# Kernel optimization log

Measured on AMD Instinct MI355X. Metric: run time of the kernel, lower is better.

The kernel has to match this reference:

```python
import jax, jax.numpy as jnp
import numpy as np

NEG_SLOPE = 0.2
BN_EPS = 1e-5
SM_EPS = 1e-16


def gatv2_conv(x, src, dst, num_nodes, Wl, bl, Wr, br, att, bias, concat):
    # x: [N, Fin]; att: [H, C]
    H, C = att.shape
    xl = (x @ Wl + bl).reshape(-1, H, C)  # source-side (x_j), lin_l
    xr = (x @ Wr + br).reshape(-1, H, C)  # target-side (x_i), lin_r
    e = jax.nn.leaky_relu(xl[src] + xr[dst], NEG_SLOPE)          # [E, H, C]
    logits = jnp.einsum('ehc,hc->eh', e, att)                    # [E, H]
    m = jax.ops.segment_max(logits, dst, num_segments=num_nodes)  # [N, H]
    expv = jnp.exp(logits - m[dst])
    denom = jax.ops.segment_sum(expv, dst, num_segments=num_nodes)
    alpha = expv / (denom[dst] + SM_EPS)                          # [E, H]
    msg = xl[src] * alpha[:, :, None]                             # [E, H, C]
    out = jax.ops.segment_sum(msg, dst, num_segments=num_nodes)   # [N, H, C]
    out = out.reshape(num_nodes, H * C) if concat else out.mean(axis=1)
    return out + bias


def batchnorm(x, gamma, beta):
    mean = x.mean(axis=0)
    var = x.var(axis=0)  # biased, as torch uses for normalization
    return gamma * (x - mean) * jax.lax.rsqrt(var + BN_EPS) + beta


def setup_inputs() -> dict:
    key = jax.random.key(0)
    ks = jax.random.split(key, 16)
    N, E = 50000, 800000
    Fin, Hid, Out, H = 128, 64, 64, 4
    s = 0.05
    inp = {
        'x': jax.random.normal(ks[0], (N, Fin), jnp.float32),
        'edge_index': jax.random.randint(ks[1], (2, E), 0, N, jnp.int64),
        # conv1 (heads=4, concat=False)
        'Wl1': jax.random.normal(ks[2], (Fin, H * Hid), jnp.float32) * s,
        'bl1': jnp.zeros((H * Hid,), jnp.float32),
        'Wr1': jax.random.normal(ks[3], (Fin, H * Hid), jnp.float32) * s,
        'br1': jnp.zeros((H * Hid,), jnp.float32),
        'att1': jax.random.normal(ks[4], (H, Hid), jnp.float32) * s,
        'bias1': jnp.zeros((Hid,), jnp.float32),
        'g1': jnp.ones((Hid,), jnp.float32),
        'beta1': jnp.zeros((Hid,), jnp.float32),
        # conv2 (heads=1, concat=True -> same as single head)
        'Wl2': jax.random.normal(ks[5], (Hid, Out), jnp.float32) * s,
        'bl2': jnp.zeros((Out,), jnp.float32),
        'Wr2': jax.random.normal(ks[6], (Hid, Out), jnp.float32) * s,
        'br2': jnp.zeros((Out,), jnp.float32),
        'att2': jax.random.normal(ks[7], (1, Out), jnp.float32) * s,
        'bias2': jnp.zeros((Out,), jnp.float32),
        'g2': jnp.ones((Out,), jnp.float32),
        'beta2': jnp.zeros((Out,), jnp.float32),
    }
    return inp


def reference(x, edge_index, Wl1, bl1, Wr1, br1, att1, bias1, g1, beta1,
              Wl2, bl2, Wr2, br2, att2, bias2, g2, beta2):
    N = x.shape[0]
    loops = jnp.arange(N, dtype=edge_index.dtype)  # PyG add_self_loops=True
    src = jnp.concatenate([edge_index[0], loops])
    dst = jnp.concatenate([edge_index[1], loops])
    h = gatv2_conv(x, src, dst, N, Wl1, bl1, Wr1, br1, att1, bias1, concat=False)
    h = jax.nn.relu(batchnorm(h, g1, beta1))  # dropout = identity (eval)
    h = gatv2_conv(h, src, dst, N, Wl2, bl2, Wr2, br2, att2, bias2, concat=True)
    h = jax.nn.relu(batchnorm(h, g2, beta2))
    return h
```

## Files before the change

kernel.cpp:

```cpp
#include <hip/hip_runtime.h>
#include <hip/hip_bf16.h>
#include <math.h>

#define TPB 256

typedef __attribute__((ext_vector_type(8))) short bfrag8;
typedef __attribute__((ext_vector_type(4))) float f32x4;

static __device__ __forceinline__ float bf2f(unsigned int u) {
  union { unsigned int i; float f; } c; c.i = u << 16; return c.f;
}
static __device__ __forceinline__ unsigned short f2bf(float f) {
  union { float f; unsigned int i; } c; c.f = f;
  unsigned int lsb = (c.i >> 16) & 1u;
  return (unsigned short)((c.i + 0x7fffu + lsb) >> 16);
}
static __device__ __forceinline__ float lrelu(float v) {
  return v > 0.f ? v : 0.2f * v;
}

__global__ void k_deg(const int* __restrict__ ei, int E, int ET, int* __restrict__ deg) {
  int e = blockIdx.x * blockDim.x + threadIdx.x;
  if (e >= ET) return;
  int dst = (e < E) ? ei[E + e] : (e - E);
  atomicAdd(&deg[dst], 1);
}

__global__ void k_scan1(const int* __restrict__ deg, int N, int* __restrict__ bsum) {
  __shared__ int sm[TPB];
  int i = blockIdx.x * TPB + threadIdx.x;
  sm[threadIdx.x] = (i < N) ? deg[i] : 0;
  __syncthreads();
  for (int d = TPB / 2; d > 0; d >>= 1) {
    if (threadIdx.x < d) sm[threadIdx.x] += sm[threadIdx.x + d];
    __syncthreads();
  }
  if (threadIdx.x == 0) bsum[blockIdx.x] = sm[0];
}

__global__ void k_scan2(const int* __restrict__ bsum, int SB, int* __restrict__ bpre,
                        int* __restrict__ rowoff, int N) {
  __shared__ int sm[TPB];
  int v = (threadIdx.x < SB) ? bsum[threadIdx.x] : 0;
  sm[threadIdx.x] = v;
  __syncthreads();
  for (int d = 1; d < TPB; d <<= 1) {
    int t = (threadIdx.x >= d) ? sm[threadIdx.x - d] : 0;
    __syncthreads();
    sm[threadIdx.x] += t;
    __syncthreads();
  }
  if (threadIdx.x < SB) bpre[threadIdx.x] = sm[threadIdx.x] - v;
  if (threadIdx.x == SB - 1) rowoff[N] = sm[SB - 1];
}

__global__ void k_scan3(const int* __restrict__ deg, const int* __restrict__ bpre,
                        int N, int* __restrict__ rowoff, int* __restrict__ cursor) {
  __shared__ int sm[TPB];
  int i = blockIdx.x * TPB + threadIdx.x;
  int v = (i < N) ? deg[i] : 0;
  sm[threadIdx.x] = v;
  __syncthreads();
  for (int d = 1; d < TPB; d <<= 1) {
    int t = (threadIdx.x >= d) ? sm[threadIdx.x - d] : 0;
    __syncthreads();
    sm[threadIdx.x] += t;
    __syncthreads();
  }
  if (i < N) {
    int off = bpre[blockIdx.x] + sm[threadIdx.x] - v;
    rowoff[i] = off;
    cursor[i] = off;
  }
}

__global__ void k_fill(const int* __restrict__ ei, int E, int ET,
                       int* __restrict__ cursor, int* __restrict__ csrc) {
  int e = blockIdx.x * blockDim.x + threadIdx.x;
  if (e >= ET) return;
  int src, dst;
  if (e < E) { src = ei[e]; dst = ei[E + e]; } else { src = dst = e - E; }
  int pos = atomicAdd(&cursor[dst], 1);
  csrc[pos] = src;
}

__global__ void k_gemm_mfma(const float* __restrict__ A,
                            const float* __restrict__ W0, const float* __restrict__ b0,
                            const float* __restrict__ W1, const float* __restrict__ b1,
                            unsigned short* __restrict__ out0, unsigned short* __restrict__ out1,
                            int M, int K, int Nc, const float* __restrict__ affine) {
  __shared__ short As[64 * 128];
  __shared__ short Bls[64 * 128];
  __shared__ short Brs[64 * 128];
  const int r0 = blockIdx.x * 64, n0 = blockIdx.y * 64;
  const int tid = threadIdx.x;
  const int Kb = K * 2;

  const int kq = K >> 2;
  for (int idx = tid; idx < 16 * K; idx += TPB) {
    int row = idx / kq, c4 = idx - row * kq;
    int gr = r0 + row;
    float4 v = make_float4(0.f, 0.f, 0.f, 0.f);
    if (gr < M) v = *(const float4*)(A + (size_t)gr * K + c4 * 4);
    if (affine) {
      int c = c4 * 4;
      v.x = fmaxf(v.x * affine[c + 0] + affine[64 + c + 0], 0.f);
      v.y = fmaxf(v.y * affine[c + 1] + affine[64 + c + 1], 0.f);
      v.z = fmaxf(v.z * affine[c + 2] + affine[64 + c + 2], 0.f);
      v.w = fmaxf(v.w * affine[c + 3] + affine[64 + c + 3], 0.f);
    }
    ushort4 pk; pk.x = f2bf(v.x); pk.y = f2bf(v.y); pk.z = f2bf(v.z); pk.w = f2bf(v.w);
    int kb = (c4 * 8) ^ ((row & 7) << 4);
    *(ushort4*)((char*)As + row * Kb + kb) = pk;
  }
  for (int idx = tid; idx < 16 * K; idx += TPB) {
    int c = idx & 63, k4 = (idx >> 6) << 2;
    const float* p0 = W0 + (size_t)k4 * Nc + n0 + c;
    const float* p1 = W1 + (size_t)k4 * Nc + n0 + c;
    ushort4 pk0, pk1;
    pk0.x = f2bf(p0[0]); pk0.y = f2bf(p0[Nc]); pk0.z = f2bf(p0[2 * Nc]); pk0.w = f2bf(p0[3 * Nc]);
    pk1.x = f2bf(p1[0]); pk1.y = f2bf(p1[Nc]); pk1.z = f2bf(p1[2 * Nc]); pk1.w = f2bf(p1[3 * Nc]);
    int kb = (k4 * 2) ^ ((c & 7) << 4);
    *(ushort4*)((char*)Bls + c * Kb + kb) = pk0;
    *(ushort4*)((char*)Brs + c * Kb + kb) = pk1;
  }
  __syncthreads();

  const int w = tid >> 6, lane = tid & 63;
  const int arow = w * 16 + (lane & 15);
  const int l16 = (lane >> 4) << 3;
  f32x4 accL[4], accR[4];
#pragma unroll
  for (int i = 0; i < 4; ++i) { accL[i] = (f32x4)0.f; accR[i] = (f32x4)0.f; }
  for (int k0 = 0; k0 < K; k0 += 32) {
    int kb = (k0 + l16) * 2;
    bfrag8 af = *(bfrag8*)((char*)As + arow * Kb + (kb ^ ((arow & 7) << 4)));
#pragma unroll
    for (int cf = 0; cf < 4; ++cf) {
      int col = cf * 16 + (lane & 15);
      int cb = col * Kb + (kb ^ ((col & 7) << 4));
      bfrag8 bl = *(bfrag8*)((char*)Bls + cb);
      accL[cf] = __builtin_amdgcn_mfma_f32_16x16x32_bf16(af, bl, accL[cf], 0, 0, 0);
      bfrag8 br = *(bfrag8*)((char*)Brs + cb);
      accR[cf] = __builtin_amdgcn_mfma_f32_16x16x32_bf16(af, br, accR[cf], 0, 0, 0);
    }
  }
  const int rbase = r0 + w * 16 + ((lane >> 4) << 2);
  const int cbase = n0 + (lane & 15);
#pragma unroll
  for (int cf = 0; cf < 4; ++cf) {
    int gcol = cbase + cf * 16;
    float bb0 = b0[gcol], bb1 = b1[gcol];
#pragma unroll
    for (int r = 0; r < 4; ++r) {
      int grow = rbase + r;
      if (grow < M) {
        out0[(size_t)grow * Nc + gcol] = f2bf(accL[cf][r] + bb0);
        out1[(size_t)grow * Nc + gcol] = f2bf(accR[cf][r] + bb1);
      }
    }
  }
}

__global__ void k_gat1(const unsigned short* __restrict__ xl,
                       const unsigned short* __restrict__ xr,
                       const int* __restrict__ rowoff, const int* __restrict__ csrc,
                       const float* __restrict__ att, const float* __restrict__ bias,
                       float* __restrict__ out, int N) {
  int node = (blockIdx.x * blockDim.x + threadIdx.x) >> 6;
  int lane = threadIdx.x & 63;
  if (node >= N) return;
  int l4 = lane * 4;
  uint2 rv = *(const uint2*)(xr + (size_t)node * 256 + l4);
  float xr0 = bf2f(rv.x & 0xffffu), xr1 = bf2f(rv.x >> 16);
  float xr2 = bf2f(rv.y & 0xffffu), xr3 = bf2f(rv.y >> 16);
  float4 at = *(const float4*)(att + l4);
  int beg = rowoff[node], end = rowoff[node + 1];
  float s = 0.f, a0 = 0.f, a1 = 0.f, a2 = 0.f, a3 = 0.f;
  int k = beg;
  for (; k + 4 <= end; k += 4) {
    int srcs[4];
#pragma unroll
    for (int u = 0; u < 4; ++u) srcs[u] = csrc[k + u];
    uint2 vv[4];
#pragma unroll
    for (int u = 0; u < 4; ++u) vv[u] = *(const uint2*)(xl + (size_t)srcs[u] * 256 + l4);
    float xs[4][4], ps[4];
#pragma unroll
    for (int u = 0; u < 4; ++u) {
      xs[u][0] = bf2f(vv[u].x & 0xffffu); xs[u][1] = bf2f(vv[u].x >> 16);
      xs[u][2] = bf2f(vv[u].y & 0xffffu); xs[u][3] = bf2f(vv[u].y >> 16);
      ps[u] = lrelu(xs[u][0] + xr0) * at.x + lrelu(xs[u][1] + xr1) * at.y
            + lrelu(xs[u][2] + xr2) * at.z + lrelu(xs[u][3] + xr3) * at.w;
    }
#pragma unroll
    for (int u = 0; u < 4; ++u) {
      ps[u] += __shfl_xor(ps[u], 1); ps[u] += __shfl_xor(ps[u], 2);
      ps[u] += __shfl_xor(ps[u], 4); ps[u] += __shfl_xor(ps[u], 8);
    }
#pragma unroll
    for (int u = 0; u < 4; ++u) {
      float w = __expf(ps[u]);
      s += w;
      a0 += w * xs[u][0]; a1 += w * xs[u][1];
      a2 += w * xs[u][2]; a3 += w * xs[u][3];
    }
  }
  for (; k < end; ++k) {
    int src = csrc[k];
    uint2 v = *(const uint2*)(xl + (size_t)src * 256 + l4);
    float x0 = bf2f(v.x & 0xffffu), x1 = bf2f(v.x >> 16);
    float x2 = bf2f(v.y & 0xffffu), x3 = bf2f(v.y >> 16);
    float p = lrelu(x0 + xr0) * at.x + lrelu(x1 + xr1) * at.y
            + lrelu(x2 + xr2) * at.z + lrelu(x3 + xr3) * at.w;
    p += __shfl_xor(p, 1); p += __shfl_xor(p, 2);
    p += __shfl_xor(p, 4); p += __shfl_xor(p, 8);
    float w = __expf(p);
    s += w;
    a0 += w * x0; a1 += w * x1; a2 += w * x2; a3 += w * x3;
  }
  float inv = 1.f / (s + 1e-16f);
  a0 *= inv; a1 *= inv; a2 *= inv; a3 *= inv;
  a0 += __shfl_xor(a0, 16); a0 += __shfl_xor(a0, 32);
  a1 += __shfl_xor(a1, 16); a1 += __shfl_xor(a1, 32);
  a2 += __shfl_xor(a2, 16); a2 += __shfl_xor(a2, 32);
  a3 += __shfl_xor(a3, 16); a3 += __shfl_xor(a3, 32);
  if (lane < 16) {
    float4 o;
    o.x = a0 * 0.25f + bias[l4 + 0];
    o.y = a1 * 0.25f + bias[l4 + 1];
    o.z = a2 * 0.25f + bias[l4 + 2];
    o.w = a3 * 0.25f + bias[l4 + 3];
    *(float4*)(out + (size_t)node * 64 + l4) = o;
  }
}

__global__ void k_gat2(const unsigned short* __restrict__ xl,
                       const unsigned short* __restrict__ xr,
                       const int* __restrict__ rowoff, const int* __restrict__ csrc,
                       const float* __restrict__ att, const float* __restrict__ bias,
                       float* __restrict__ out, int N) {
  int node = (blockIdx.x * blockDim.x + threadIdx.x) >> 6;
  int lane = threadIdx.x & 63;
  if (node >= N) return;
  int grp = lane >> 4, c4 = (lane & 15) * 4;
  uint2 rv = *(const uint2*)(xr + (size_t)node * 64 + c4);
  float xr0 = bf2f(rv.x & 0xffffu), xr1 = bf2f(rv.x >> 16);
  float xr2 = bf2f(rv.y & 0xffffu), xr3 = bf2f(rv.y >> 16);
  float4 at = *(const float4*)(att + c4);
  int beg = rowoff[node], end = rowoff[node + 1];
  int iters = (end - beg + 3) >> 2;
  float s = 0.f, a0 = 0.f, a1 = 0.f, a2 = 0.f, a3 = 0.f;
  for (int it = 0; it < iters; ++it) {
    int kk = beg + it * 4 + grp;
    bool ok = kk < end;
    int src = ok ? csrc[kk] : 0;
    uint2 v = *(const uint2*)(xl + (size_t)src * 64 + c4);
    float x0 = bf2f(v.x & 0xffffu), x1 = bf2f(v.x >> 16);
    float x2 = bf2f(v.y & 0xffffu), x3 = bf2f(v.y >> 16);
    float p = lrelu(x0 + xr0) * at.x + lrelu(x1 + xr1) * at.y
            + lrelu(x2 + xr2) * at.z + lrelu(x3 + xr3) * at.w;
    p += __shfl_xor(p, 1); p += __shfl_xor(p, 2);
    p += __shfl_xor(p, 4); p += __shfl_xor(p, 8);
    float w = ok ? __expf(p) : 0.f;
    s += w;
    a0 += w * x0; a1 += w * x1; a2 += w * x2; a3 += w * x3;
  }
  s  += __shfl_xor(s, 16);  s  += __shfl_xor(s, 32);
  a0 += __shfl_xor(a0, 16); a0 += __shfl_xor(a0, 32);
  a1 += __shfl_xor(a1, 16); a1 += __shfl_xor(a1, 32);
  a2 += __shfl_xor(a2, 16); a2 += __shfl_xor(a2, 32);
  a3 += __shfl_xor(a3, 16); a3 += __shfl_xor(a3, 32);
  if (lane < 16) {
    float inv = 1.f / (s + 1e-16f);
    float4 o;
    o.x = a0 * inv + bias[c4 + 0];
    o.y = a1 * inv + bias[c4 + 1];
    o.z = a2 * inv + bias[c4 + 2];
    o.w = a3 * inv + bias[c4 + 3];
    *(float4*)(out + (size_t)node * 64 + c4) = o;
  }
}

__global__ void k_bnstat(const float* __restrict__ in, int N, float* __restrict__ part) {
  __shared__ float sm[TPB], sq[TPB];
  int col = threadIdx.x & 63;
  int rq = threadIdx.x >> 6;
  float s = 0.f, q = 0.f;
  for (int r = blockIdx.x * 4 + rq; r < N; r += gridDim.x * 4) {
    float v = in[(size_t)r * 64 + col];
    s += v; q += v * v;
  }
  sm[threadIdx.x] = s; sq[threadIdx.x] = q;
  __syncthreads();
  if (threadIdx.x < 64) {
    s = sm[threadIdx.x] + sm[threadIdx.x + 64] + sm[threadIdx.x + 128] + sm[threadIdx.x + 192];
    q = sq[threadIdx.x] + sq[threadIdx.x + 64] + sq[threadIdx.x + 128] + sq[threadIdx.x + 192];
    part[(size_t)blockIdx.x * 128 + threadIdx.x] = s;
    part[(size_t)blockIdx.x * 128 + 64 + threadIdx.x] = q;
  }
}

__global__ void k_bnfin(const float* __restrict__ part, int B, int N,
                        const float* __restrict__ g, const float* __restrict__ beta,
                        float* __restrict__ ab) {
  int c = threadIdx.x;
  float s = 0.f, q = 0.f;
  for (int b = 0; b < B; ++b) {
    s += part[(size_t)b * 128 + c];
    q += part[(size_t)b * 128 + 64 + c];
  }
  float mean = s / (float)N;
  float var = q / (float)N - mean * mean;
  float a = g[c] * rsqrtf(var + 1e-5f);
  ab[c] = a;
  ab[64 + c] = beta[c] - mean * a;
}

__global__ void k_bnapply(const float* __restrict__ in, const float* __restrict__ ab,
                          float* __restrict__ out, int total4) {
  int idx = blockIdx.x * blockDim.x + threadIdx.x;
  if (idx >= total4) return;
  float4 v = *(const float4*)(in + (size_t)idx * 4);
  int c0 = (idx & 15) * 4;
  v.x = fmaxf(v.x * ab[c0 + 0] + ab[64 + c0 + 0], 0.f);
  v.y = fmaxf(v.y * ab[c0 + 1] + ab[64 + c0 + 1], 0.f);
  v.z = fmaxf(v.z * ab[c0 + 2] + ab[64 + c0 + 2], 0.f);
  v.w = fmaxf(v.w * ab[c0 + 3] + ab[64 + c0 + 3], 0.f);
  *(float4*)(out + (size_t)idx * 4) = v;
}

extern "C" void kernel_launch(void* const* d_in, const int* in_sizes, int n_in,
                              void* d_out, int out_size, void* d_ws, size_t ws_size,
                              hipStream_t stream) {
  const float* x     = (const float*)d_in[0];
  const int*   ei    = (const int*)d_in[1];
  const float* Wl1   = (const float*)d_in[2];
  const float* bl1   = (const float*)d_in[3];
  const float* Wr1   = (const float*)d_in[4];
  const float* br1   = (const float*)d_in[5];
  const float* att1  = (const float*)d_in[6];
  const float* bias1 = (const float*)d_in[7];
  const float* g1    = (const float*)d_in[8];
  const float* be1   = (const float*)d_in[9];
  const float* Wl2   = (const float*)d_in[10];
  const float* bl2   = (const float*)d_in[11];
  const float* Wr2   = (const float*)d_in[12];
  const float* br2   = (const float*)d_in[13];
  const float* att2  = (const float*)d_in[14];
  const float* bias2 = (const float*)d_in[15];
  const float* g2    = (const float*)d_in[16];
  const float* be2   = (const float*)d_in[17];
  float* out = (float*)d_out;

  const int N  = in_sizes[0] / 128;
  const int E  = in_sizes[1] / 2;
  const int ET = E + N;
  const int SB = (N + TPB - 1) / TPB;

  char* p = (char*)d_ws;
  auto take = [&](size_t b) { char* q = p; p += (b + 255) & ~(size_t)255; return q; };

  unsigned short* xl1 = (unsigned short*)take((size_t)N * 256 * 2);
  unsigned short* xr1 = (unsigned short*)take((size_t)N * 256 * 2);
  unsigned short* xl2 = (unsigned short*)take((size_t)N * 64 * 2);
  unsigned short* xr2 = (unsigned short*)take((size_t)N * 64 * 2);
  float* out1 = (float*)take((size_t)N * 64 * 4);
  int* deg    = (int*)take((size_t)N * 4);
  int* rowoff = (int*)take((size_t)(N + 1) * 4);
  int* cursor = (int*)take((size_t)N * 4);
  int* csrc   = (int*)take((size_t)ET * 4);
  int* bsum   = (int*)take((size_t)SB * 4);
  int* bpre   = (int*)take((size_t)SB * 4);
  float* part = (float*)take((size_t)128 * 128 * 4);
  float* ab1  = (float*)take(128 * 4);
  float* ab2  = (float*)take(128 * 4);
  (void)ws_size; (void)n_in; (void)out_size;

  int egrid = (ET + TPB - 1) / TPB;
  int ngrid = (N + 3) / 4;
  int mtile = (N + 63) / 64;
  int total4 = N * 16;

  hipMemsetAsync(deg, 0, (size_t)N * 4, stream);
  k_deg<<<egrid, TPB, 0, stream>>>(ei, E, ET, deg);
  k_scan1<<<SB, TPB, 0, stream>>>(deg, N, bsum);
  k_scan2<<<1, TPB, 0, stream>>>(bsum, SB, bpre, rowoff, N);
  k_scan3<<<SB, TPB, 0, stream>>>(deg, bpre, N, rowoff, cursor);
  k_fill<<<egrid, TPB, 0, stream>>>(ei, E, ET, cursor, csrc);

  k_gemm_mfma<<<dim3(mtile, 4), TPB, 0, stream>>>(x, Wl1, bl1, Wr1, br1, xl1, xr1,
                                                  N, 128, 256, nullptr);
  k_gat1<<<ngrid, TPB, 0, stream>>>(xl1, xr1, rowoff, csrc, att1, bias1, out1, N);
  k_bnstat<<<128, TPB, 0, stream>>>(out1, N, part);
  k_bnfin<<<1, 64, 0, stream>>>(part, 128, N, g1, be1, ab1);

  k_gemm_mfma<<<dim3(mtile, 1), TPB, 0, stream>>>(out1, Wl2, bl2, Wr2, br2, xl2, xr2,
                                                  N, 64, 64, ab1);
  k_gat2<<<ngrid, TPB, 0, stream>>>(xl2, xr2, rowoff, csrc, att2, bias2, out, N);
  k_bnstat<<<128, TPB, 0, stream>>>(out, N, part);
  k_bnfin<<<1, 64, 0, stream>>>(part, 128, N, g2, be2, ab2);
  k_bnapply<<<(total4 + TPB - 1) / TPB, TPB, 0, stream>>>(out, ab2, out, total4);
}
```

Measured before the change: 406.9 us.

## Pad CSR rows to multiples of four, pre-transpose weights, restructure GEMM and GAT kernels

Weight matrices are now converted once to transposed bf16 inside the degree-count kernel. Each GEMM block loads its A tile once and loops over all output column tiles, instead of launching separate column blocks that reload A and convert weights. CSR rows are padded to a multiple of four so the GAT kernels can use int4 index loads and a masked tail, and the separate scan2 kernel is removed by having each scan3 block reduce the prior block sums itself. Lane reductions use DPP row rotates instead of shuffles, and the bnstat grid is doubled. In exchange, padding needs a larger zeroed csrc buffer, and the GEMM with K=128 now runs fewer blocks, each doing serial column loops.

```diff
diff --git a/kernel.cpp b/kernel.cpp
--- a/kernel.cpp
+++ b/kernel.cpp
@@ -15,21 +15,52 @@
   unsigned int lsb = (c.i >> 16) & 1u;
   return (unsigned short)((c.i + 0x7fffu + lsb) >> 16);
 }
-static __device__ __forceinline__ float lrelu(float v) {
-  return v > 0.f ? v : 0.2f * v;
-}
-
-__global__ void k_deg(const int* __restrict__ ei, int E, int ET, int* __restrict__ deg) {
-  int e = blockIdx.x * blockDim.x + threadIdx.x;
-  if (e >= ET) return;
-  int dst = (e < E) ? ei[E + e] : (e - E);
-  atomicAdd(&deg[dst], 1);
+
+#define DPP_ROR(v, C) __int_as_float(__builtin_amdgcn_update_dpp( \
+    __float_as_int(v), __float_as_int(v), (C), 0xf, 0xf, false))
+static __device__ __forceinline__ float red16(float p) {
+  p += DPP_ROR(p, 0x121);
+  p += DPP_ROR(p, 0x122);
+  p += DPP_ROR(p, 0x124);
+  p += DPP_ROR(p, 0x128);
+  return p;
+}
+
+__global__ void k_deg_prep(const int* __restrict__ ei, int E, int ET, int* __restrict__ deg,
+                           const float* __restrict__ Wl1, const float* __restrict__ Wr1,
+                           const float* __restrict__ Wl2, const float* __restrict__ Wr2,
+                           unsigned short* __restrict__ wt1l, unsigned short* __restrict__ wt1r,
+                           unsigned short* __restrict__ wt2l, unsigned short* __restrict__ wt2r,
+                           int egrid) {
+  int b = blockIdx.x;
+  if (b < egrid) {
+    int e = b * TPB + threadIdx.x;
+    if (e < ET) {
+      int dst = (e < E) ? ei[E + e] : (e - E);
+      atomicAdd(&deg[dst], 1);
+    }
+  } else {
+    int i = (b - egrid) * TPB + threadIdx.x;
+    if (i < 32768) {
+      int c = i >> 7, k = i & 127;
+      wt1l[i] = f2bf(Wl1[(size_t)k * 256 + c]);
+    } else if (i < 65536) {
+      int j = i - 32768; int c = j >> 7, k = j & 127;
+      wt1r[j] = f2bf(Wr1[(size_t)k * 256 + c]);
+    } else if (i < 69632) {
+      int j = i - 65536; int c = j >> 6, k = j & 63;
+      wt2l[j] = f2bf(Wl2[(size_t)k * 64 + c]);
+    } else if (i < 73728) {
+      int j = i - 69632; int c = j >> 6, k = j & 63;
+      wt2r[j] = f2bf(Wr2[(size_t)k * 64 + c]);
+    }
+  }
 }
 
 __global__ void k_scan1(const int* __restrict__ deg, int N, int* __restrict__ bsum) {
   __shared__ int sm[TPB];
   int i = blockIdx.x * TPB + threadIdx.x;
-  sm[threadIdx.x] = (i < N) ? deg[i] : 0;
+  sm[threadIdx.x] = (i < N) ? ((deg[i] + 3) & ~3) : 0;
   __syncthreads();
   for (int d = TPB / 2; d > 0; d >>= 1) {
     if (threadIdx.x < d) sm[threadIdx.x] += sm[threadIdx.x + d];
@@ -38,37 +69,30 @@
   if (threadIdx.x == 0) bsum[blockIdx.x] = sm[0];
 }
 
-__global__ void k_scan2(const int* __restrict__ bsum, int SB, int* __restrict__ bpre,
-                        int* __restrict__ rowoff, int N) {
+__global__ void k_scan3(const int* __restrict__ deg, const int* __restrict__ bsum,
+                        int SB, int N, int* __restrict__ rowoff, int* __restrict__ cursor) {
   __shared__ int sm[TPB];
-  int v = (threadIdx.x < SB) ? bsum[threadIdx.x] : 0;
+  int pv = (threadIdx.x < blockIdx.x) ? bsum[threadIdx.x] : 0;
+  sm[threadIdx.x] = pv;
+  __syncthreads();
+  for (int dd = TPB / 2; dd > 0; dd >>= 1) {
+    if (threadIdx.x < dd) sm[threadIdx.x] += sm[threadIdx.x + dd];
+    __syncthreads();
+  }
+  int base = sm[0];
+  __syncthreads();
+  int i = blockIdx.x * TPB + threadIdx.x;
+  int v = (i < N) ? ((deg[i] + 3) & ~3) : 0;
   sm[threadIdx.x] = v;
   __syncthreads();
-  for (int d = 1; d < TPB; d <<= 1) {
-    int t = (threadIdx.x >= d) ? sm[threadIdx.x - d] : 0;
+  for (int dd = 1; dd < TPB; dd <<= 1) {
+    int t = (threadIdx.x >= dd) ? sm[threadIdx.x - dd] : 0;
     __syncthreads();
     sm[threadIdx.x] += t;
     __syncthreads();
   }
-  if (threadIdx.x < SB) bpre[threadIdx.x] = sm[threadIdx.x] - v;
-  if (threadIdx.x == SB - 1) rowoff[N] = sm[SB - 1];
-}
-
-__global__ void k_scan3(const int* __restrict__ deg, const int* __restrict__ bpre,
-                        int N, int* __restrict__ rowoff, int* __restrict__ cursor) {
-  __shared__ int sm[TPB];
-  int i = blockIdx.x * TPB + threadIdx.x;
-  int v = (i < N) ? deg[i] : 0;
-  sm[threadIdx.x] = v;
-  __syncthreads();
-  for (int d = 1; d < TPB; d <<= 1) {
-    int t = (threadIdx.x >= d) ? sm[threadIdx.x - d] : 0;
-    __syncthreads();
-    sm[threadIdx.x] += t;
-    __syncthreads();
-  }
   if (i < N) {
-    int off = bpre[blockIdx.x] + sm[threadIdx.x] - v;
+    int off = base + sm[threadIdx.x] - v;
     rowoff[i] = off;
     cursor[i] = off;
   }
@@ -84,21 +108,26 @@
   csrc[pos] = src;
 }
 
-__global__ void k_gemm_mfma(const float* __restrict__ A,
-                            const float* __restrict__ W0, const float* __restrict__ b0,
-                            const float* __restrict__ W1, const float* __restrict__ b1,
+__global__ void k_gemm_mfma(const float* __restrict__ A, const float* __restrict__ affine,
+                            const unsigned short* __restrict__ Wt0, const float* __restrict__ b0,
+                            const unsigned short* __restrict__ Wt1, const float* __restrict__ b1,
                             unsigned short* __restrict__ out0, unsigned short* __restrict__ out1,
-                            int M, int K, int Nc, const float* __restrict__ affine) {
-  __shared__ short As[64 * 128];
-  __shared__ short Bls[64 * 128];
-  __shared__ short Brs[64 * 128];
-  const int r0 = blockIdx.x * 64, n0 = blockIdx.y * 64;
+                            int M, int K, int Nc) {
+  extern __shared__ short lds[];
+  short* As = lds;
+  short* Bls = lds + 64 * K;
+  short* Brs = lds + 128 * K;
+  const int r0 = blockIdx.x * 64;
   const int tid = threadIdx.x;
   const int Kb = K * 2;
-
-  const int kq = K >> 2;
-  for (int idx = tid; idx < 16 * K; idx += TPB) {
-    int row = idx / kq, c4 = idx - row * kq;
+  const int w = tid >> 6, lane = tid & 63;
+  const int arow = w * 16 + (lane & 15);
+  const int l16 = (lane >> 4) << 3;
+  const int rbase0 = r0 + w * 16 + ((lane >> 4) << 2);
+
+  const int fpr = K >> 2;
+  for (int idx = tid; idx < 64 * fpr; idx += TPB) {
+    int row = idx / fpr, c4 = idx - row * fpr;
     int gr = r0 + row;
     float4 v = make_float4(0.f, 0.f, 0.f, 0.f);
     if (gr < M) v = *(const float4*)(A + (size_t)gr * K + c4 * 4);
@@ -113,111 +142,127 @@
     int kb = (c4 * 8) ^ ((row & 7) << 4);
     *(ushort4*)((char*)As + row * Kb + kb) = pk;
   }
-  for (int idx = tid; idx < 16 * K; idx += TPB) {
-    int c = idx & 63, k4 = (idx >> 6) << 2;
-    const float* p0 = W0 + (size_t)k4 * Nc + n0 + c;
-    const float* p1 = W1 + (size_t)k4 * Nc + n0 + c;
-    ushort4 pk0, pk1;
-    pk0.x = f2bf(p0[0]); pk0.y = f2bf(p0[Nc]); pk0.z = f2bf(p0[2 * Nc]); pk0.w = f2bf(p0[3 * Nc]);
-    pk1.x = f2bf(p1[0]); pk1.y = f2bf(p1[Nc]); pk1.z = f2bf(p1[2 * Nc]); pk1.w = f2bf(p1[3 * Nc]);
-    int kb = (k4 * 2) ^ ((c & 7) << 4);
-    *(ushort4*)((char*)Bls + c * Kb + kb) = pk0;
-    *(ushort4*)((char*)Brs + c * Kb + kb) = pk1;
-  }
-  __syncthreads();
-
-  const int w = tid >> 6, lane = tid & 63;
-  const int arow = w * 16 + (lane & 15);
-  const int l16 = (lane >> 4) << 3;
-  f32x4 accL[4], accR[4];
-#pragma unroll
-  for (int i = 0; i < 4; ++i) { accL[i] = (f32x4)0.f; accR[i] = (f32x4)0.f; }
-  for (int k0 = 0; k0 < K; k0 += 32) {
-    int kb = (k0 + l16) * 2;
-    bfrag8 af = *(bfrag8*)((char*)As + arow * Kb + (kb ^ ((arow & 7) << 4)));
+
+  const int cpr = K >> 3;
+  for (int nt = 0; nt < Nc; nt += 64) {
+    __syncthreads();
+    for (int idx = tid; idx < 64 * cpr; idx += TPB) {
+      int c = idx / cpr, k8 = (idx - c * cpr) * 8;
+      int kb = (k8 * 2) ^ ((c & 7) << 4);
+      uint4 w0 = *(const uint4*)(Wt0 + (size_t)(nt + c) * K + k8);
+      *(uint4*)((char*)Bls + c * Kb + kb) = w0;
+      uint4 w1 = *(const uint4*)(Wt1 + (size_t)(nt + c) * K + k8);
+      *(uint4*)((char*)Brs + c * Kb + kb) = w1;
+    }
+    __syncthreads();
+
+    f32x4 accL[4], accR[4];
+#pragma unroll
+    for (int i = 0; i < 4; ++i) { accL[i] = (f32x4)0.f; accR[i] = (f32x4)0.f; }
+    for (int k0 = 0; k0 < K; k0 += 32) {
+      int kb = (k0 + l16) * 2;
+      bfrag8 af = *(bfrag8*)((char*)As + arow * Kb + (kb ^ ((arow & 7) << 4)));
+#pragma unroll
+      for (int cf = 0; cf < 4; ++cf) {
+        int col = cf * 16 + (lane & 15);
+        int cb = col * Kb + (kb ^ ((col & 7) << 4));
+        bfrag8 bl = *(bfrag8*)((char*)Bls + cb);
+        accL[cf] = __builtin_amdgcn_mfma_f32_16x16x32_bf16(af, bl, accL[cf], 0, 0, 0);
+        bfrag8 br = *(bfrag8*)((char*)Brs + cb);
+        accR[cf] = __builtin_amdgcn_mfma_f32_16x16x32_bf16(af, br, accR[cf], 0, 0, 0);
+      }
+    }
+    const int cbase = nt + (lane & 15);
 #pragma unroll
     for (int cf = 0; cf < 4; ++cf) {
-      int col = cf * 16 + (lane & 15);
-      int cb = col * Kb + (kb ^ ((col & 7) << 4));
-      bfrag8 bl = *(bfrag8*)((char*)Bls + cb);
-      accL[cf] = __builtin_amdgcn_mfma_f32_16x16x32_bf16(af, bl, accL[cf], 0, 0, 0);
-      bfrag8 br = *(bfrag8*)((char*)Brs + cb);
-      accR[cf] = __builtin_amdgcn_mfma_f32_16x16x32_bf16(af, br, accR[cf], 0, 0, 0);
-    }
-  }
-  const int rbase = r0 + w * 16 + ((lane >> 4) << 2);
-  const int cbase = n0 + (lane & 15);
-#pragma unroll
-  for (int cf = 0; cf < 4; ++cf) {
-    int gcol = cbase + cf * 16;
-    float bb0 = b0[gcol], bb1 = b1[gcol];
-#pragma unroll
-    for (int r = 0; r < 4; ++r) {
-      int grow = rbase + r;
-      if (grow < M) {
-        out0[(size_t)grow * Nc + gcol] = f2bf(accL[cf][r] + bb0);
-        out1[(size_t)grow * Nc + gcol] = f2bf(accR[cf][r] + bb1);
+      int gcol = cbase + cf * 16;
+      float bb0 = b0[gcol], bb1 = b1[gcol];
+#pragma unroll
+      for (int r = 0; r < 4; ++r) {
+        int grow = rbase0 + r;
+        if (grow < M) {
+          out0[(size_t)grow * Nc + gcol] = f2bf(accL[cf][r] + bb0);
+          out1[(size_t)grow * Nc + gcol] = f2bf(accR[cf][r] + bb1);
+        }
       }
     }
   }
 }
 
-__global__ void k_gat1(const unsigned short* __restrict__ xl,
-                       const unsigned short* __restrict__ xr,
-                       const int* __restrict__ rowoff, const int* __restrict__ csrc,
-                       const float* __restrict__ att, const float* __restrict__ bias,
-                       float* __restrict__ out, int N) {
-  int node = (blockIdx.x * blockDim.x + threadIdx.x) >> 6;
+__global__ __launch_bounds__(TPB) void k_gat1(
+    const unsigned short* __restrict__ xl, const unsigned short* __restrict__ xr,
+    const int* __restrict__ rowoff, const int* __restrict__ deg,
+    const int* __restrict__ csrc,
+    const float* __restrict__ att, const float* __restrict__ bias,
+    float* __restrict__ out, int N) {
+  int node = (blockIdx.x * TPB + threadIdx.x) >> 6;
   int lane = threadIdx.x & 63;
   if (node >= N) return;
   int l4 = lane * 4;
-  uint2 rv = *(const uint2*)(xr + (size_t)node * 256 + l4);
+  float4 atv = *(const float4*)(att + l4);
+  float4 bb = *(const float4*)(bias + l4);
+  uint2 rv = *(const uint2*)(xr + (node << 8) + l4);
   float xr0 = bf2f(rv.x & 0xffffu), xr1 = bf2f(rv.x >> 16);
   float xr2 = bf2f(rv.y & 0xffffu), xr3 = bf2f(rv.y >> 16);
-  float4 at = *(const float4*)(att + l4);
-  int beg = rowoff[node], end = rowoff[node + 1];
+  int beg = rowoff[node];
+  int dg = deg[node];
+  int endR = beg + dg;
+  int endF = beg + (dg & ~3);
   float s = 0.f, a0 = 0.f, a1 = 0.f, a2 = 0.f, a3 = 0.f;
   int k = beg;
-  for (; k + 4 <= end; k += 4) {
-    int srcs[4];
-#pragma unroll
-    for (int u = 0; u < 4; ++u) srcs[u] = csrc[k + u];
+  for (; k < endF; k += 4) {
+    int4 q = *(const int4*)(csrc + k);
     uint2 vv[4];
-#pragma unroll
-    for (int u = 0; u < 4; ++u) vv[u] = *(const uint2*)(xl + (size_t)srcs[u] * 256 + l4);
+    vv[0] = *(const uint2*)(xl + (q.x << 8) + l4);
+    vv[1] = *(const uint2*)(xl + (q.y << 8) + l4);
+    vv[2] = *(const uint2*)(xl + (q.z << 8) + l4);
+    vv[3] = *(const uint2*)(xl + (q.w << 8) + l4);
     float xs[4][4], ps[4];
 #pragma unroll
     for (int u = 0; u < 4; ++u) {
       xs[u][0] = bf2f(vv[u].x & 0xffffu); xs[u][1] = bf2f(vv[u].x >> 16);
       xs[u][2] = bf2f(vv[u].y & 0xffffu); xs[u][3] = bf2f(vv[u].y >> 16);
-      ps[u] = lrelu(xs[u][0] + xr0) * at.x + lrelu(xs[u][1] + xr1) * at.y
-            + lrelu(xs[u][2] + xr2) * at.z + lrelu(xs[u][3] + xr3) * at.w;
-    }
+      float t0 = xs[u][0] + xr0, t1 = xs[u][1] + xr1;
+      float t2 = xs[u][2] + xr2, t3 = xs[u][3] + xr3;
+      ps[u] = fmaxf(t0, 0.2f * t0) * atv.x + fmaxf(t1, 0.2f * t1) * atv.y
+            + fmaxf(t2, 0.2f * t2) * atv.z + fmaxf(t3, 0.2f * t3) * atv.w;
+    }
+#pragma unroll
+    for (int u = 0; u < 4; ++u) ps[u] = red16(ps[u]);
 #pragma unroll
     for (int u = 0; u < 4; ++u) {
-      ps[u] += __shfl_xor(ps[u], 1); ps[u] += __shfl_xor(ps[u], 2);
-      ps[u] += __shfl_xor(ps[u], 4); ps[u] += __shfl_xor(ps[u], 8);
-    }
+      float wv = __expf(ps[u]);
+      s += wv;
+      a0 += wv * xs[u][0]; a1 += wv * xs[u][1];
+      a2 += wv * xs[u][2]; a3 += wv * xs[u][3];
+    }
+  }
+  if (k < endR) {
+    int4 q = *(const int4*)(csrc + k);
+    uint2 vv[4];
+    vv[0] = *(const uint2*)(xl + (q.x << 8) + l4);
+    vv[1] = *(const uint2*)(xl + (q.y << 8) + l4);
+    vv[2] = *(const uint2*)(xl + (q.z << 8) + l4);
+    vv[3] = *(const uint2*)(xl + (q.w << 8) + l4);
+    float xs[4][4], ps[4];
 #pragma unroll
     for (int u = 0; u < 4; ++u) {
-      float w = __expf(ps[u]);
-      s += w;
-      a0 += w * xs[u][0]; a1 += w * xs[u][1];
-      a2 += w * xs[u][2]; a3 += w * xs[u][3];
-    }
-  }
-  for (; k < end; ++k) {
-    int src = csrc[k];
-    uint2 v = *(const uint2*)(xl + (size_t)src * 256 + l4);
-    float x0 = bf2f(v.x & 0xffffu), x1 = bf2f(v.x >> 16);
-    float x2 = bf2f(v.y & 0xffffu), x3 = bf2f(v.y >> 16);
-    float p = lrelu(x0 + xr0) * at.x + lrelu(x1 + xr1) * at.y
-            + lrelu(x2 + xr2) * at.z + lrelu(x3 + xr3) * at.w;
-    p += __shfl_xor(p, 1); p += __shfl_xor(p, 2);
-    p += __shfl_xor(p, 4); p += __shfl_xor(p, 8);
-    float w = __expf(p);
-    s += w;
-    a0 += w * x0; a1 += w * x1; a2 += w * x2; a3 += w * x3;
+      xs[u][0] = bf2f(vv[u].x & 0xffffu); xs[u][1] = bf2f(vv[u].x >> 16);
+      xs[u][2] = bf2f(vv[u].y & 0xffffu); xs[u][3] = bf2f(vv[u].y >> 16);
+      float t0 = xs[u][0] + xr0, t1 = xs[u][1] + xr1;
+      float t2 = xs[u][2] + xr2, t3 = xs[u][3] + xr3;
+      ps[u] = fmaxf(t0, 0.2f * t0) * atv.x + fmaxf(t1, 0.2f * t1) * atv.y
+            + fmaxf(t2, 0.2f * t2) * atv.z + fmaxf(t3, 0.2f * t3) * atv.w;
+    }
+#pragma unroll
+    for (int u = 0; u < 4; ++u) ps[u] = red16(ps[u]);
+#pragma unroll
+    for (int u = 0; u < 4; ++u) {
+      float wv = (k + u < endR) ? __expf(ps[u]) : 0.f;
+      s += wv;
+      a0 += wv * xs[u][0]; a1 += wv * xs[u][1];
+      a2 += wv * xs[u][2]; a3 += wv * xs[u][3];
+    }
   }
   float inv = 1.f / (s + 1e-16f);
   a0 *= inv; a1 *= inv; a2 *= inv; a3 *= inv;
@@ -227,46 +272,50 @@
   a3 += __shfl_xor(a3, 16); a3 += __shfl_xor(a3, 32);
   if (lane < 16) {
     float4 o;
-    o.x = a0 * 0.25f + bias[l4 + 0];
-    o.y = a1 * 0.25f + bias[l4 + 1];
-    o.z = a2 * 0.25f + bias[l4 + 2];
-    o.w = a3 * 0.25f + bias[l4 + 3];
-    *(float4*)(out + (size_t)node * 64 + l4) = o;
-  }
-}
-
-__global__ void k_gat2(const unsigned short* __restrict__ xl,
-                       const unsigned short* __restrict__ xr,
-                       const int* __restrict__ rowoff, const int* __restrict__ csrc,
-                       const float* __restrict__ att, const float* __restrict__ bias,
-                       float* __restrict__ out, int N) {
-  int node = (blockIdx.x * blockDim.x + threadIdx.x) >> 6;
+    o.x = a0 * 0.25f + bb.x;
+    o.y = a1 * 0.25f + bb.y;
+    o.z = a2 * 0.25f + bb.z;
+    o.w = a3 * 0.25f + bb.w;
+    *(float4*)(out + (node << 6) + l4) = o;
+  }
+}
+
+__global__ __launch_bounds__(TPB) void k_gat2(
+    const unsigned short* __restrict__ xl, const unsigned short* __restrict__ xr,
+    const int* __restrict__ rowoff, const int* __restrict__ deg,
+    const int* __restrict__ csrc,
+    const float* __restrict__ att, const float* __restrict__ bias,
+    float* __restrict__ out, int N) {
+  int node = (blockIdx.x * TPB + threadIdx.x) >> 6;
   int lane = threadIdx.x & 63;
   if (node >= N) return;
   int grp = lane >> 4, c4 = (lane & 15) * 4;
-  uint2 rv = *(const uint2*)(xr + (size_t)node * 64 + c4);
+  float4 atv = *(const float4*)(att + c4);
+  float4 bb = *(const float4*)(bias + c4);
+  uint2 rv = *(const uint2*)(xr + (node << 6) + c4);
   float xr0 = bf2f(rv.x & 0xffffu), xr1 = bf2f(rv.x >> 16);
   float xr2 = bf2f(rv.y & 0xffffu), xr3 = bf2f(rv.y >> 16);
-  float4 at = *(const float4*)(att + c4);
-  int beg = rowoff[node], end = rowoff[node + 1];
-  int iters = (end - beg + 3) >> 2;
+  int beg = rowoff[node];
+  int dg = deg[node];
+  int endR = beg + dg;
+  int quads = (dg + 3) >> 2;
   float s = 0.f, a0 = 0.f, a1 = 0.f, a2 = 0.f, a3 = 0.f;
-  for (int it = 0; it < iters; ++it) {
+  for (int it = 0; it < quads; ++it) {
     int kk = beg + it * 4 + grp;
-    bool ok = kk < end;
-    int src = ok ? csrc[kk] : 0;
-    uint2 v = *(const uint2*)(xl + (size_t)src * 64 + c4);
+    int src = csrc[kk];
+    bool ok = kk < endR;
+    uint2 v = *(const uint2*)(xl + (src << 6) + c4);
     float x0 = bf2f(v.x & 0xffffu), x1 = bf2f(v.x >> 16);
     float x2 = bf2f(v.y & 0xffffu), x3 = bf2f(v.y >> 16);
-    float p = lrelu(x0 + xr0) * at.x + lrelu(x1 + xr1) * at.y
-            + lrelu(x2 + xr2) * at.z + lrelu(x3 + xr3) * at.w;
-    p += __shfl_xor(p, 1); p += __shfl_xor(p, 2);
-    p += __shfl_xor(p, 4); p += __shfl_xor(p, 8);
-    float w = ok ? __expf(p) : 0.f;
-    s += w;
-    a0 += w * x0; a1 += w * x1; a2 += w * x2; a3 += w * x3;
-  }
-  s  += __shfl_xor(s, 16);  s  += __shfl_xor(s, 32);
+    float t0 = x0 + xr0, t1 = x1 + xr1, t2 = x2 + xr2, t3 = x3 + xr3;
+    float p = fmaxf(t0, 0.2f * t0) * atv.x + fmaxf(t1, 0.2f * t1) * atv.y
+            + fmaxf(t2, 0.2f * t2) * atv.z + fmaxf(t3, 0.2f * t3) * atv.w;
+    p = red16(p);
+    float wv = ok ? __expf(p) : 0.f;
+    s += wv;
+    a0 += wv * x0; a1 += wv * x1; a2 += wv * x2; a3 += wv * x3;
+  }
+  s += __shfl_xor(s, 16); s += __shfl_xor(s, 32);
   a0 += __shfl_xor(a0, 16); a0 += __shfl_xor(a0, 32);
   a1 += __shfl_xor(a1, 16); a1 += __shfl_xor(a1, 32);
   a2 += __shfl_xor(a2, 16); a2 += __shfl_xor(a2, 32);
@@ -274,11 +323,11 @@
   if (lane < 16) {
     float inv = 1.f / (s + 1e-16f);
     float4 o;
-    o.x = a0 * inv + bias[c4 + 0];
-    o.y = a1 * inv + bias[c4 + 1];
-    o.z = a2 * inv + bias[c4 + 2];
-    o.w = a3 * inv + bias[c4 + 3];
-    *(float4*)(out + (size_t)node * 64 + c4) = o;
+    o.x = a0 * inv + bb.x;
+    o.y = a1 * inv + bb.y;
+    o.z = a2 * inv + bb.z;
+    o.w = a3 * inv + bb.w;
+    *(float4*)(out + (node << 6) + c4) = o;
   }
 }
 
@@ -356,6 +405,7 @@
   const int N  = in_sizes[0] / 128;
   const int E  = in_sizes[1] / 2;
   const int ET = E + N;
+  const int ETP = ET + 4 * ((N + 255) & ~255);
   const int SB = (N + TPB - 1) / TPB;
 
   char* p = (char*)d_ws;
@@ -366,39 +416,45 @@
   unsigned short* xl2 = (unsigned short*)take((size_t)N * 64 * 2);
   unsigned short* xr2 = (unsigned short*)take((size_t)N * 64 * 2);
   float* out1 = (float*)take((size_t)N * 64 * 4);
+  unsigned short* wt1l = (unsigned short*)take(256 * 128 * 2);
+  unsigned short* wt1r = (unsigned short*)take(256 * 128 * 2);
+  unsigned short* wt2l = (unsigned short*)take(64 * 64 * 2);
+  unsigned short* wt2r = (unsigned short*)take(64 * 64 * 2);
   int* deg    = (int*)take((size_t)N * 4);
+  int* csrc   = (int*)take((size_t)ETP * 4 + 16);
+  size_t zero_bytes = (char*)(csrc + ETP) + 16 - (char*)deg;
   int* rowoff = (int*)take((size_t)(N + 1) * 4);
   int* cursor = (int*)take((size_t)N * 4);
-  int* csrc   = (int*)take((size_t)ET * 4);
   int* bsum   = (int*)take((size_t)SB * 4);
-  int* bpre   = (int*)take((size_t)SB * 4);
-  float* part = (float*)take((size_t)128 * 128 * 4);
+  float* part = (float*)take((size_t)256 * 128 * 4);
   float* ab1  = (float*)take(128 * 4);
   float* ab2  = (float*)take(128 * 4);
   (void)ws_size; (void)n_in; (void)out_size;
 
   int egrid = (ET + TPB - 1) / TPB;
+  int wgrid = (73728 + TPB - 1) / TPB;
   int ngrid = (N + 3) / 4;
   int mtile = (N + 63) / 64;
   int total4 = N * 16;
 
-  hipMemsetAsync(deg, 0, (size_t)N * 4, stream);
-  k_deg<<<egrid, TPB, 0, stream>>>(ei, E, ET, deg);
+  hipMemsetAsync(deg, 0, zero_bytes, stream);
+  k_deg_prep<<<egrid + wgrid, TPB, 0, stream>>>(ei, E, ET, deg,
+                                                Wl1, Wr1, Wl2, Wr2,
+                                                wt1l, wt1r, wt2l, wt2r, egrid);
   k_scan1<<<SB, TPB, 0, stream>>>(deg, N, bsum);
-  k_scan2<<<1, TPB, 0, stream>>>(bsum, SB, bpre, rowoff, N);
-  k_scan3<<<SB, TPB, 0, stream>>>(deg, bpre, N, rowoff, cursor);
+  k_scan3<<<SB, TPB, 0, stream>>>(deg, bsum, SB, N, rowoff, cursor);
   k_fill<<<egrid, TPB, 0, stream>>>(ei, E, ET, cursor, csrc);
 
-  k_gemm_mfma<<<dim3(mtile, 4), TPB, 0, stream>>>(x, Wl1, bl1, Wr1, br1, xl1, xr1,
-                                                  N, 128, 256, nullptr);
-  k_gat1<<<ngrid, TPB, 0, stream>>>(xl1, xr1, rowoff, csrc, att1, bias1, out1, N);
-  k_bnstat<<<128, TPB, 0, stream>>>(out1, N, part);
-  k_bnfin<<<1, 64, 0, stream>>>(part, 128, N, g1, be1, ab1);
-
-  k_gemm_mfma<<<dim3(mtile, 1), TPB, 0, stream>>>(out1, Wl2, bl2, Wr2, br2, xl2, xr2,
-                                                  N, 64, 64, ab1);
-  k_gat2<<<ngrid, TPB, 0, stream>>>(xl2, xr2, rowoff, csrc, att2, bias2, out, N);
-  k_bnstat<<<128, TPB, 0, stream>>>(out, N, part);
-  k_bnfin<<<1, 64, 0, stream>>>(part, 128, N, g2, be2, ab2);
+  k_gemm_mfma<<<mtile, TPB, 3 * 64 * 128 * 2, stream>>>(
+      x, nullptr, wt1l, bl1, wt1r, br1, xl1, xr1, N, 128, 256);
+  k_gat1<<<ngrid, TPB, 0, stream>>>(xl1, xr1, rowoff, deg, csrc, att1, bias1, out1, N);
+  k_bnstat<<<256, TPB, 0, stream>>>(out1, N, part);
+  k_bnfin<<<1, 64, 0, stream>>>(part, 256, N, g1, be1, ab1);
+
+  k_gemm_mfma<<<mtile, TPB, 3 * 64 * 64 * 2, stream>>>(
+      out1, ab1, wt2l, bl2, wt2r, br2, xl2, xr2, N, 64, 64);
+  k_gat2<<<ngrid, TPB, 0, stream>>>(xl2, xr2, rowoff, deg, csrc, att2, bias2, out, N);
+  k_bnstat<<<256, TPB, 0, stream>>>(out, N, part);
+  k_bnfin<<<1, 64, 0, stream>>>(part, 256, N, g2, be2, ab2);
   k_bnapply<<<(total4 + TPB - 1) / TPB, TPB, 0, stream>>>(out, ab2, out, total4);
 }
```

Result: slower. 423.6 us (+4.1%).
